# Performance work log

Measured on AMD Instinct MI355X. Metric: run time of the kernel, lower is better.

Reference implementation:

```python
import jax, jax.numpy as jnp
import numpy as np

B, N, S, K, R = 4, 8192, 2048, 64, 0.2  # batch, points, centroids, neighbors, ball radius
EPS = 1e-5  # BatchNorm eps


def fps_indices(x, n_samples):
    """Farthest point sampling; returns int32 [B, n_samples] indices."""
    xs = jax.lax.stop_gradient(x)
    Bb, Nn, _ = xs.shape

    def step(carry, _):
        dist, farthest = carry
        centroid = jnp.take_along_axis(xs, farthest[:, None, None], axis=1)  # [B,1,3]
        d = jnp.sum((xs - centroid) ** 2, axis=-1)  # [B,N]
        dist = jnp.minimum(dist, d)
        nxt = jnp.argmax(dist, axis=-1).astype(jnp.int32)
        return (dist, nxt), farthest

    init = (jnp.full((Bb, Nn), 1e10, xs.dtype), jnp.zeros((Bb,), jnp.int32))
    _, idxs = jax.lax.scan(step, init, None, length=n_samples)  # [S,B]
    return jnp.transpose(idxs)  # [B,S]


def ball_query(x, centroids, radius, k):
    """First k point indices within radius of each centroid, -1 padded. int32 [B,S,k]."""
    xs = jax.lax.stop_gradient(x)
    cs = jax.lax.stop_gradient(centroids)
    Nn = xs.shape[1]
    d2 = jnp.sum((cs[:, :, None, :] - xs[:, None, :, :]) ** 2, axis=-1)  # [B,S,N]
    cand = jnp.where(d2 < radius * radius, jnp.arange(Nn, dtype=jnp.int32), Nn)
    neg_topk, _ = jax.lax.top_k(-cand, k)  # k smallest candidate indices
    idx = -neg_topk
    return jnp.where(idx == Nn, -1, idx)


def _forward(x, x_complete, layers, idx_fps, idx_ball):
    centroids = jnp.take_along_axis(x, idx_fps[..., None], axis=1)  # [B,S,3]
    valid = idx_ball >= 0  # [B,S,K]
    sidx = jnp.maximum(idx_ball, 0)
    gather = lambda pts: jax.vmap(lambda p, i: p[i])(pts, sidx)  # [B,S,K,C]
    x_local = gather(x) - centroids[:, :, None, :]  # relative coords
    feats = jnp.concatenate([gather(x_complete), x_local], axis=-1)  # [B,S,K,67]
    h = feats.reshape(B, S * K, -1).transpose(0, 2, 1)  # [B,67,S*K]
    for (W, b, g, bt, m, v) in layers:  # Conv1d(k=1) -> BN(eval) -> ReLU
        h = jnp.einsum('oc,bcn->bon', W, h) + b[None, :, None]
        h = (h - m[None, :, None]) * (g * jax.lax.rsqrt(v + EPS))[None, :, None] + bt[None, :, None]
        h = jax.nn.relu(h)
    h = h.reshape(B, -1, S, K)  # [B,128,S,K]
    h = jnp.where(valid[:, None, :, :], h, -jnp.inf)  # mask invalid neighbors
    pooled = jnp.max(h, axis=3)  # masked max pool over neighborhood
    return centroids, pooled.transpose(0, 2, 1)  # [B,S,3], [B,S,128]


def setup_inputs():
    key = jax.random.key(0)
    ks = jax.random.split(key, 8)
    x = jax.random.uniform(ks[0], (B, N, 3), jnp.float32)
    x_complete = jax.random.normal(ks[1], (B, N, 64), jnp.float32)
    dims = [67, 64, 64, 128]
    inp = {'x': x, 'x_complete': x_complete}
    for i in range(3):
        cin, cout = dims[i], dims[i + 1]
        kk = jax.random.split(ks[2 + i], 6)
        inp[f'W{i+1}'] = jax.random.normal(kk[0], (cout, cin), jnp.float32) * 0.05
        inp[f'b{i+1}'] = jax.random.normal(kk[1], (cout,), jnp.float32) * 0.02
        inp[f'g{i+1}'] = 1.0 + 0.1 * jax.random.normal(kk[2], (cout,), jnp.float32)
        inp[f'bt{i+1}'] = jax.random.normal(kk[3], (cout,), jnp.float32) * 0.02
        inp[f'm{i+1}'] = jax.random.normal(kk[4], (cout,), jnp.float32) * 0.05
        inp[f'v{i+1}'] = jax.random.uniform(kk[5], (cout,), jnp.float32, minval=0.5, maxval=1.5)
    return inp


def reference(x, x_complete, W1, b1, g1, bt1, m1, v1, W2, b2, g2, bt2, m2, v2, W3, b3, g3, bt3, m3, v3):
    idx_fps = fps_indices(x, S)
    cen_sg = jnp.take_along_axis(jax.lax.stop_gradient(x), idx_fps[..., None], axis=1)
    idx_ball = ball_query(x, cen_sg, R, K)
    layers = ((W1, b1, g1, bt1, m1, v1), (W2, b2, g2, bt2, m2, v2), (W3, b3, g3, bt3, m3, v3))
    return _forward(x, x_complete, layers, idx_fps, idx_ball)
```

## Files before the change

kernel.cpp:

```cpp
#include <hip/hip_runtime.h>
#include <math.h>

#define BATCH 4
#define NPTS  8192
#define NSAMP 2048
#define KNBR  64
#define EPSF  1e-5f

__global__ void prep_kernel(const float* __restrict__ W1, const float* __restrict__ W2,
                            const float* __restrict__ W3,
                            float* __restrict__ W1t, float* __restrict__ W2t,
                            float* __restrict__ W3t) {
    int t = threadIdx.x;
    for (int i = t; i < 64 * 67; i += 256) { int o = i / 67, c = i % 67; W1t[c * 64 + o] = W1[i]; }
    for (int i = t; i < 64 * 64; i += 256) { int o = i >> 6, c = i & 63; W2t[c * 64 + o] = W2[i]; }
    for (int i = t; i < 128 * 64; i += 256) { int o = i >> 6, c = i & 63; W3t[c * 128 + o] = W3[i]; }
}

#define DPP_FMAX(v, ctrl)                                                            \
    do {                                                                             \
        int _t = __builtin_amdgcn_update_dpp(0, __float_as_int(v), ctrl, 0xf, 0xf, true); \
        (v) = fmaxf((v), __int_as_float(_t));                                        \
    } while (0)

__global__ __launch_bounds__(512, 2) void fps_kernel(const float* __restrict__ x,
                                                     float* __restrict__ cen_out) {
#pragma clang fp contract(off)
    const int tid = threadIdx.x;
    const int lane = tid & 63;
    const int wid = tid >> 6;
    __shared__ float4 sp[NPTS];
    __shared__ __align__(16) unsigned long long pub[2][8];
    __shared__ int hist[NSAMP];

    const float* xb = x + (size_t)blockIdx.x * NPTS * 3;
    for (int i = tid; i < NPTS; i += 512) {
        sp[i] = (float4){xb[3 * i + 0], xb[3 * i + 1], xb[3 * i + 2], 0.f};
    }
    __syncthreads();

    float qx[16], qy[16], qz[16], dist[16];
    const int base = tid * 16;
#pragma unroll
    for (int i = 0; i < 16; i++) {
        float4 a = sp[base + i];
        qx[i] = a.x; qy[i] = a.y; qz[i] = a.z;
        dist[i] = 1e10f;
    }

    int cur = 0;
    float4 cp = sp[0];
    for (int s = 0; s < NSAMP; s++) {
        if (tid == 0) hist[s] = cur;
        const float cx = cp.x, cy = cp.y, cz = cp.z;
        float ta0 = -1.f, ta1 = -1.f, ta2 = -1.f, ta3 = -1.f;
#pragma unroll
        for (int i = 0; i < 16; i++) {
            float dx = qx[i] - cx;
            float dy = qy[i] - cy;
            float dz = qz[i] - cz;
            float d = ((dx * dx) + (dy * dy)) + (dz * dz);
            float dm = fminf(dist[i], d);
            dist[i] = dm;
            if ((i & 3) == 0) ta0 = fmaxf(ta0, dm);
            if ((i & 3) == 1) ta1 = fmaxf(ta1, dm);
            if ((i & 3) == 2) ta2 = fmaxf(ta2, dm);
            if ((i & 3) == 3) ta3 = fmaxf(ta3, dm);
        }
        float bestd = fmaxf(fmaxf(ta0, ta1), fmaxf(ta2, ta3));

        float w = bestd;
        DPP_FMAX(w, 0x111);
        DPP_FMAX(w, 0x112);
        DPP_FMAX(w, 0x114);
        DPP_FMAX(w, 0x118);
        DPP_FMAX(w, 0x142);
        DPP_FMAX(w, 0x143);
        const float wmax = __int_as_float(__builtin_amdgcn_readlane(__float_as_int(w), 63));

        unsigned long long mask = __ballot(bestd == wmax);
        int wl = (int)__builtin_ctzll(mask);

        int c[16];
#pragma unroll
        for (int i = 0; i < 16; i++) c[i] = (dist[i] == wmax) ? i : 0x7fffffff;
        int m0 = min(min(c[0], c[1]), c[2]);
        int m1 = min(min(c[3], c[4]), c[5]);
        int m2 = min(min(c[6], c[7]), c[8]);
        int m3 = min(min(c[9], c[10]), c[11]);
        int m4 = min(min(c[12], c[13]), c[14]);
        int lo5 = min(min(m0, m1), m2);
        int lo6 = min(min(m3, m4), c[15]);
        int lo = min(lo5, lo6);

        int lwin = __builtin_amdgcn_readlane(lo, wl);
        int widx = (wid << 10) + (wl << 4) + lwin;
        unsigned long long key =
            ((unsigned long long)__float_as_uint(wmax) << 32) |
            (unsigned)(NPTS - 1 - widx);

        const int p = s & 1;
        if (lane == 63) pub[p][wid] = key;
        __syncthreads();

        unsigned long long q0 = pub[p][0], q1 = pub[p][1];
        unsigned long long q2 = pub[p][2], q3 = pub[p][3];
        unsigned long long q4 = pub[p][4], q5 = pub[p][5];
        unsigned long long q6 = pub[p][6], q7 = pub[p][7];
        unsigned long long a0 = q0 > q1 ? q0 : q1;
        unsigned long long a1 = q2 > q3 ? q2 : q3;
        unsigned long long a2 = q4 > q5 ? q4 : q5;
        unsigned long long a3 = q6 > q7 ? q6 : q7;
        unsigned long long b0 = a0 > a1 ? a0 : a1;
        unsigned long long b1 = a2 > a3 ? a2 : a3;
        unsigned long long kbest = b0 > b1 ? b0 : b1;
        cur = (NPTS - 1) - (int)(unsigned)kbest;
        cp = sp[cur];
    }

    __syncthreads();
    for (int i = tid; i < NSAMP; i += 512) {
        int idx = hist[i];
        float4 q = sp[idx];
        float* o = cen_out + ((size_t)blockIdx.x * NSAMP + i) * 3;
        o[0] = q.x; o[1] = q.y; o[2] = q.z;
    }
}

__global__ __launch_bounds__(256) void ball_kernel(const float* __restrict__ x,
                                                   const float* __restrict__ cen,
                                                   int* __restrict__ idxb) {
    const int wid = threadIdx.x >> 6, lane = threadIdx.x & 63;
    const int id = blockIdx.x * 4 + wid;
    const int b = id >> 11;
    const float r2 = (float)(0.2 * 0.2);
    const float cx = cen[3 * id], cy = cen[3 * id + 1], cz = cen[3 * id + 2];
    const float* xb = x + (size_t)b * NPTS * 3;

    int count = 0;
    for (int base = 0; base < NPTS && count < KNBR; base += 64) {
        int p = base + lane;
        float pxv = xb[3 * p], pyv = xb[3 * p + 1], pzv = xb[3 * p + 2];
        float dx = __fsub_rn(cx, pxv);
        float dy = __fsub_rn(cy, pyv);
        float dz = __fsub_rn(cz, pzv);
        float d2 = __fadd_rn(__fadd_rn(__fmul_rn(dx, dx), __fmul_rn(dy, dy)), __fmul_rn(dz, dz));
        bool hit = d2 < r2;
        unsigned long long m = __ballot(hit);
        if (hit) {
            int pos = count + __popcll(m & ((1ull << lane) - 1ull));
            if (pos < KNBR) idxb[(size_t)id * KNBR + pos] = p;
        }
        count += (int)__popcll(m);
    }
    for (int pos = count + lane; pos < KNBR; pos += 64)
        idxb[(size_t)id * KNBR + pos] = -1;
}

__global__ __launch_bounds__(256) void mlp_kernel(
    const float* __restrict__ x, const float* __restrict__ xc,
    const float* __restrict__ cen, const int* __restrict__ idxb,
    const float* __restrict__ W1t, const float* __restrict__ b1, const float* __restrict__ g1,
    const float* __restrict__ bt1, const float* __restrict__ m1, const float* __restrict__ v1,
    const float* __restrict__ W2t, const float* __restrict__ b2, const float* __restrict__ g2,
    const float* __restrict__ bt2, const float* __restrict__ m2, const float* __restrict__ v2,
    const float* __restrict__ W3t, const float* __restrict__ b3, const float* __restrict__ g3,
    const float* __restrict__ bt3, const float* __restrict__ m3, const float* __restrict__ v3,
    float* __restrict__ pooled) {
    const int wid = threadIdx.x >> 6, lane = threadIdx.x & 63;
    const int id = blockIdx.x * 4 + wid;
    const int b = id >> 11;
    __shared__ float sred[4][64][33];

    int il = idxb[(size_t)id * KNBR + lane];
    bool valid = il >= 0;
    int ik = valid ? il : 0;

    float cx = cen[3 * id], cy = cen[3 * id + 1], cz = cen[3 * id + 2];
    const float* xp = x + ((size_t)b * NPTS + ik) * 3;
    const float* xcp = xc + ((size_t)b * NPTS + ik) * 64;

    float h1[64];
#pragma unroll
    for (int o = 0; o < 64; o++) h1[o] = 0.f;
#pragma unroll
    for (int c4 = 0; c4 < 16; c4++) {
        float4 t = ((const float4*)xcp)[c4];
        float tv0 = t.x, tv1 = t.y, tv2 = t.z, tv3 = t.w;
#pragma unroll
        for (int o = 0; o < 64; o++) h1[o] = fmaf(W1t[(c4 * 4 + 0) * 64 + o], tv0, h1[o]);
#pragma unroll
        for (int o = 0; o < 64; o++) h1[o] = fmaf(W1t[(c4 * 4 + 1) * 64 + o], tv1, h1[o]);
#pragma unroll
        for (int o = 0; o < 64; o++) h1[o] = fmaf(W1t[(c4 * 4 + 2) * 64 + o], tv2, h1[o]);
#pragma unroll
        for (int o = 0; o < 64; o++) h1[o] = fmaf(W1t[(c4 * 4 + 3) * 64 + o], tv3, h1[o]);
    }
    {
        float xl0 = xp[0] - cx, xl1 = xp[1] - cy, xl2 = xp[2] - cz;
#pragma unroll
        for (int o = 0; o < 64; o++) h1[o] = fmaf(W1t[64 * 64 + o], xl0, h1[o]);
#pragma unroll
        for (int o = 0; o < 64; o++) h1[o] = fmaf(W1t[65 * 64 + o], xl1, h1[o]);
#pragma unroll
        for (int o = 0; o < 64; o++) h1[o] = fmaf(W1t[66 * 64 + o], xl2, h1[o]);
    }
#pragma unroll
    for (int o = 0; o < 64; o++) {
        float sc = g1[o] * rsqrtf(v1[o] + EPSF);
        h1[o] = fmaxf(fmaf(h1[o] + b1[o] - m1[o], sc, bt1[o]), 0.f);
    }

    float h2[64];
#pragma unroll
    for (int o = 0; o < 64; o++) h2[o] = 0.f;
#pragma unroll
    for (int c = 0; c < 64; c++) {
        float hv = h1[c];
#pragma unroll
        for (int o = 0; o < 64; o++) h2[o] = fmaf(W2t[c * 64 + o], hv, h2[o]);
    }
#pragma unroll
    for (int o = 0; o < 64; o++) {
        float sc = g2[o] * rsqrtf(v2[o] + EPSF);
        h2[o] = fmaxf(fmaf(h2[o] + b2[o] - m2[o], sc, bt2[o]), 0.f);
    }

    for (int ch = 0; ch < 4; ch++) {
        float acc[32];
#pragma unroll
        for (int oo = 0; oo < 32; oo++) acc[oo] = 0.f;
#pragma unroll
        for (int c = 0; c < 64; c++) {
            float hv = h2[c];
#pragma unroll
            for (int oo = 0; oo < 32; oo++)
                acc[oo] = fmaf(W3t[c * 128 + ch * 32 + oo], hv, acc[oo]);
        }
#pragma unroll
        for (int oo = 0; oo < 32; oo++) {
            int o = ch * 32 + oo;
            float sc = g3[o] * rsqrtf(v3[o] + EPSF);
            float t = fmaxf(fmaf(acc[oo] + b3[o] - m3[o], sc, bt3[o]), 0.f);
            sred[wid][lane][oo] = valid ? t : -INFINITY;
        }
        __syncthreads();
        {
            int c = lane & 31, half = lane >> 5;
            float mx = -INFINITY;
#pragma unroll
            for (int r = 0; r < 32; r++) mx = fmaxf(mx, sred[wid][half * 32 + r][c]);
            mx = fmaxf(mx, __shfl_xor(mx, 32, 64));
            if (lane < 32) pooled[(size_t)id * 128 + ch * 32 + c] = mx;
        }
        __syncthreads();
    }
}

extern "C" void kernel_launch(void* const* d_in, const int* in_sizes, int n_in,
                              void* d_out, int out_size, void* d_ws, size_t ws_size,
                              hipStream_t stream) {
    const float* x  = (const float*)d_in[0];
    const float* xc = (const float*)d_in[1];
    const float* W1 = (const float*)d_in[2];
    const float* b1 = (const float*)d_in[3];
    const float* g1 = (const float*)d_in[4];
    const float* bt1 = (const float*)d_in[5];
    const float* m1 = (const float*)d_in[6];
    const float* v1 = (const float*)d_in[7];
    const float* W2 = (const float*)d_in[8];
    const float* b2 = (const float*)d_in[9];
    const float* g2 = (const float*)d_in[10];
    const float* bt2 = (const float*)d_in[11];
    const float* m2 = (const float*)d_in[12];
    const float* v2 = (const float*)d_in[13];
    const float* W3 = (const float*)d_in[14];
    const float* b3 = (const float*)d_in[15];
    const float* g3 = (const float*)d_in[16];
    const float* bt3 = (const float*)d_in[17];
    const float* m3 = (const float*)d_in[18];
    const float* v3 = (const float*)d_in[19];

    float* out = (float*)d_out;
    float* cen = out;
    float* pooled = out + (size_t)BATCH * NSAMP * 3;

    int* idxb = (int*)d_ws;
    float* W1t = (float*)((char*)d_ws + (size_t)BATCH * NSAMP * KNBR * 4);
    float* W2t = W1t + 67 * 64;
    float* W3t = W2t + 64 * 64;

    prep_kernel<<<1, 256, 0, stream>>>(W1, W2, W3, W1t, W2t, W3t);
    fps_kernel<<<BATCH, 512, 0, stream>>>(x, cen);
    ball_kernel<<<(BATCH * NSAMP) / 4, 256, 0, stream>>>(x, cen, idxb);
    mlp_kernel<<<(BATCH * NSAMP) / 4, 256, 0, stream>>>(
        x, xc, cen, idxb,
        W1t, b1, g1, bt1, m1, v1,
        W2t, b2, g2, bt2, m2, v2,
        W3t, b3, g3, bt3, m3, v3,
        pooled);
}
```

Baseline: 2.425 ms.

## Spatially sort FPS points by Morton cell and skip unaffected threads via bounding-box bound

FPS points are bucketed into an 8x8x8 Morton grid with a shared-memory histogram, prefix scan and scatter, so each thread holds a spatially compact set of 16 points. Each thread keeps a bounding box and skips its distance update when the box's lower-bound distance to the new centroid is at least its current max distance. The per-wave reduction now carries a packed 64-bit key (distance, original index, sorted position), which removes the separate argmin tie-break pass. This adds setup cost, a 64-bit DPP reduction (two DPP ops per step), and depends on inputs falling in [0,1) for the grid to cluster well; occupancy hint drops to 1 block.

```diff
diff --git a/kernel.cpp b/kernel.cpp
--- a/kernel.cpp
+++ b/kernel.cpp
@@ -17,90 +17,137 @@
     for (int i = t; i < 128 * 64; i += 256) { int o = i >> 6, c = i & 63; W3t[c * 128 + o] = W3[i]; }
 }
 
-#define DPP_FMAX(v, ctrl)                                                            \
-    do {                                                                             \
-        int _t = __builtin_amdgcn_update_dpp(0, __float_as_int(v), ctrl, 0xf, 0xf, true); \
-        (v) = fmaxf((v), __int_as_float(_t));                                        \
+#define DPP_KMAX(k, ctrl)                                                              \
+    do {                                                                               \
+        unsigned lo_ = (unsigned)(k);                                                  \
+        unsigned hi_ = (unsigned)((k) >> 32);                                          \
+        int slo_ = __builtin_amdgcn_update_dpp(0, (int)lo_, ctrl, 0xf, 0xf, true);     \
+        int shi_ = __builtin_amdgcn_update_dpp(0, (int)hi_, ctrl, 0xf, 0xf, true);     \
+        unsigned long long ks_ =                                                       \
+            ((unsigned long long)(unsigned)shi_ << 32) | (unsigned)slo_;               \
+        if (ks_ > (k)) (k) = ks_;                                                      \
     } while (0)
 
-__global__ __launch_bounds__(512, 2) void fps_kernel(const float* __restrict__ x,
+__device__ __forceinline__ unsigned spread3(unsigned v) {
+    return (v & 1u) | ((v & 2u) << 2) | ((v & 4u) << 4);
+}
+
+__global__ __launch_bounds__(512, 1) void fps_kernel(const float* __restrict__ x,
                                                      float* __restrict__ cen_out) {
 #pragma clang fp contract(off)
     const int tid = threadIdx.x;
     const int lane = tid & 63;
     const int wid = tid >> 6;
-    __shared__ float4 sp[NPTS];
+    __shared__ float4 srt[NPTS];
+    __shared__ unsigned hcnt[512];
+    __shared__ unsigned hofs[512];
+    __shared__ int hist[NSAMP];
     __shared__ __align__(16) unsigned long long pub[2][8];
-    __shared__ int hist[NSAMP];
 
     const float* xb = x + (size_t)blockIdx.x * NPTS * 3;
-    for (int i = tid; i < NPTS; i += 512) {
-        sp[i] = (float4){xb[3 * i + 0], xb[3 * i + 1], xb[3 * i + 2], 0.f};
+
+    hcnt[tid] = 0u;
+    __syncthreads();
+    unsigned mycell[16];
+#pragma unroll
+    for (int i = 0; i < 16; i++) {
+        int g = tid * 16 + i;
+        float px = xb[3 * g], py = xb[3 * g + 1], pz = xb[3 * g + 2];
+        unsigned ix = (unsigned)min(7, max(0, (int)(px * 8.f)));
+        unsigned iy = (unsigned)min(7, max(0, (int)(py * 8.f)));
+        unsigned iz = (unsigned)min(7, max(0, (int)(pz * 8.f)));
+        unsigned cell = spread3(ix) | (spread3(iy) << 1) | (spread3(iz) << 2);
+        mycell[i] = cell;
+        atomicAdd(&hcnt[cell], 1u);
+    }
+    __syncthreads();
+    {
+        unsigned own = hcnt[tid];
+        for (int d = 1; d < 512; d <<= 1) {
+            unsigned t = (tid >= d) ? hcnt[tid - d] : 0u;
+            __syncthreads();
+            hcnt[tid] += t;
+            __syncthreads();
+        }
+        hofs[tid] = hcnt[tid] - own;
+    }
+    __syncthreads();
+#pragma unroll
+    for (int i = 0; i < 16; i++) {
+        int g = tid * 16 + i;
+        unsigned pos = atomicAdd(&hofs[mycell[i]], 1u);
+        srt[pos] = (float4){xb[3 * g], xb[3 * g + 1], xb[3 * g + 2], __int_as_float(g)};
     }
     __syncthreads();
 
     float qx[16], qy[16], qz[16], dist[16];
-    const int base = tid * 16;
+    unsigned pe[16];
 #pragma unroll
     for (int i = 0; i < 16; i++) {
-        float4 a = sp[base + i];
+        float4 a = srt[tid * 16 + i];
         qx[i] = a.x; qy[i] = a.y; qz[i] = a.z;
         dist[i] = 1e10f;
-    }
-
+        unsigned orig = (unsigned)__float_as_int(a.w);
+        pe[i] = (((unsigned)(NPTS - 1) - orig) << 13) | (unsigned)(tid * 16 + i);
+    }
+    float lox = qx[0], hix = qx[0], loy = qy[0], hiy = qy[0], loz = qz[0], hiz = qz[0];
+#pragma unroll
+    for (int i = 1; i < 16; i++) {
+        lox = fminf(lox, qx[i]); hix = fmaxf(hix, qx[i]);
+        loy = fminf(loy, qy[i]); hiy = fmaxf(hiy, qy[i]);
+        loz = fminf(loz, qz[i]); hiz = fmaxf(hiz, qz[i]);
+    }
+
+    float tau = 1e10f;
+    unsigned long long myKey = 0ull;
     int cur = 0;
-    float4 cp = sp[0];
+    float cx = xb[0], cy = xb[1], cz = xb[2];
+
     for (int s = 0; s < NSAMP; s++) {
         if (tid == 0) hist[s] = cur;
-        const float cx = cp.x, cy = cp.y, cz = cp.z;
-        float ta0 = -1.f, ta1 = -1.f, ta2 = -1.f, ta3 = -1.f;
-#pragma unroll
-        for (int i = 0; i < 16; i++) {
-            float dx = qx[i] - cx;
-            float dy = qy[i] - cy;
-            float dz = qz[i] - cz;
-            float d = ((dx * dx) + (dy * dy)) + (dz * dz);
-            float dm = fminf(dist[i], d);
-            dist[i] = dm;
-            if ((i & 3) == 0) ta0 = fmaxf(ta0, dm);
-            if ((i & 3) == 1) ta1 = fmaxf(ta1, dm);
-            if ((i & 3) == 2) ta2 = fmaxf(ta2, dm);
-            if ((i & 3) == 3) ta3 = fmaxf(ta3, dm);
-        }
-        float bestd = fmaxf(fmaxf(ta0, ta1), fmaxf(ta2, ta3));
-
-        float w = bestd;
-        DPP_FMAX(w, 0x111);
-        DPP_FMAX(w, 0x112);
-        DPP_FMAX(w, 0x114);
-        DPP_FMAX(w, 0x118);
-        DPP_FMAX(w, 0x142);
-        DPP_FMAX(w, 0x143);
-        const float wmax = __int_as_float(__builtin_amdgcn_readlane(__float_as_int(w), 63));
-
-        unsigned long long mask = __ballot(bestd == wmax);
-        int wl = (int)__builtin_ctzll(mask);
-
-        int c[16];
-#pragma unroll
-        for (int i = 0; i < 16; i++) c[i] = (dist[i] == wmax) ? i : 0x7fffffff;
-        int m0 = min(min(c[0], c[1]), c[2]);
-        int m1 = min(min(c[3], c[4]), c[5]);
-        int m2 = min(min(c[6], c[7]), c[8]);
-        int m3 = min(min(c[9], c[10]), c[11]);
-        int m4 = min(min(c[12], c[13]), c[14]);
-        int lo5 = min(min(m0, m1), m2);
-        int lo6 = min(min(m3, m4), c[15]);
-        int lo = min(lo5, lo6);
-
-        int lwin = __builtin_amdgcn_readlane(lo, wl);
-        int widx = (wid << 10) + (wl << 4) + lwin;
-        unsigned long long key =
-            ((unsigned long long)__float_as_uint(wmax) << 32) |
-            (unsigned)(NPTS - 1 - widx);
+        float bx = cx - fminf(fmaxf(cx, lox), hix);
+        float by = cy - fminf(fmaxf(cy, loy), hiy);
+        float bz = cz - fminf(fmaxf(cz, loz), hiz);
+        float lb2 = ((bx * bx) + (by * by)) + (bz * bz);
+        if (lb2 < tau * 1.000002f) {
+#pragma unroll
+            for (int i = 0; i < 16; i++) {
+                float dx = qx[i] - cx;
+                float dy = qy[i] - cy;
+                float dz = qz[i] - cz;
+                float d = ((dx * dx) + (dy * dy)) + (dz * dz);
+                dist[i] = fminf(dist[i], d);
+            }
+            float u0 = fmaxf(dist[0], dist[1]),  u1 = fmaxf(dist[2], dist[3]);
+            float u2 = fmaxf(dist[4], dist[5]),  u3 = fmaxf(dist[6], dist[7]);
+            float u4 = fmaxf(dist[8], dist[9]),  u5 = fmaxf(dist[10], dist[11]);
+            float u6 = fmaxf(dist[12], dist[13]), u7 = fmaxf(dist[14], dist[15]);
+            float v0 = fmaxf(u0, u1), v1 = fmaxf(u2, u3);
+            float v2 = fmaxf(u4, u5), v3 = fmaxf(u6, u7);
+            tau = fmaxf(fmaxf(v0, v1), fmaxf(v2, v3));
+            unsigned f0 = 0u, f1 = 0u, f2 = 0u, f3 = 0u;
+#pragma unroll
+            for (int i = 0; i < 16; i += 4) {
+                f0 = max(f0, (dist[i + 0] == tau) ? pe[i + 0] : 0u);
+                f1 = max(f1, (dist[i + 1] == tau) ? pe[i + 1] : 0u);
+                f2 = max(f2, (dist[i + 2] == tau) ? pe[i + 2] : 0u);
+                f3 = max(f3, (dist[i + 3] == tau) ? pe[i + 3] : 0u);
+            }
+            unsigned fe = max(max(f0, f1), max(f2, f3));
+            myKey = ((unsigned long long)__float_as_uint(tau) << 32) |
+                    (unsigned long long)fe;
+        }
+
+        unsigned long long k = myKey;
+        DPP_KMAX(k, 0x111);
+        DPP_KMAX(k, 0x112);
+        DPP_KMAX(k, 0x114);
+        DPP_KMAX(k, 0x118);
+        DPP_KMAX(k, 0x142);
+        DPP_KMAX(k, 0x143);
 
         const int p = s & 1;
-        if (lane == 63) pub[p][wid] = key;
+        if (lane == 63) pub[p][wid] = k;
         __syncthreads();
 
         unsigned long long q0 = pub[p][0], q1 = pub[p][1];
@@ -114,16 +161,18 @@
         unsigned long long b0 = a0 > a1 ? a0 : a1;
         unsigned long long b1 = a2 > a3 ? a2 : a3;
         unsigned long long kbest = b0 > b1 ? b0 : b1;
-        cur = (NPTS - 1) - (int)(unsigned)kbest;
-        cp = sp[cur];
+
+        unsigned pos = (unsigned)kbest & 0x1FFFu;
+        cur = (NPTS - 1) - (int)((kbest >> 13) & 0x1FFFull);
+        float4 a = srt[pos];
+        cx = a.x; cy = a.y; cz = a.z;
     }
 
     __syncthreads();
     for (int i = tid; i < NSAMP; i += 512) {
         int idx = hist[i];
-        float4 q = sp[idx];
         float* o = cen_out + ((size_t)blockIdx.x * NSAMP + i) * 3;
-        o[0] = q.x; o[1] = q.y; o[2] = q.z;
+        o[0] = xb[3 * idx]; o[1] = xb[3 * idx + 1]; o[2] = xb[3 * idx + 2];
     }
 }
 
```

Measured after the change: 2.313 ms. 1.05x faster.
